# Performance work log

Hardware: AMD Instinct MI355X
Metric: run time of the kernel (lower is better)

Reference implementation:

```python
import jax, jax.numpy as jnp
import numpy as np


def _square_distance(src, dst):
    # src: [B,N,C], dst: [B,M,C] -> [B,N,M] squared euclidean distances
    # ||s-d||^2 = -2 s.d + ||s||^2 + ||d||^2
    d = -2.0 * jnp.einsum('bnc,bmc->bnm', src, dst)
    d = d + jnp.sum(src * src, axis=-1)[:, :, None]
    d = d + jnp.sum(dst * dst, axis=-1)[:, None, :]
    return d


def setup_inputs() -> dict:
    key = jax.random.key(0)
    k1, k2 = jax.random.split(key)
    B, N, M, C = 8, 4096, 4096, 3
    f = jax.random.normal(k1, (B, N, C), dtype=jnp.float32)
    f_ = jax.random.normal(k2, (B, M, C), dtype=jnp.float32)
    return {"f": f, "f_": f_}


def reference(f, f_):
    dis = _square_distance(f, f_)          # [B,N,M]
    f2f_ = jnp.min(dis, axis=2)            # [B,N] nearest in f_ for each f point
    f_2f = jnp.min(dis, axis=1)            # [B,M] nearest in f for each f_ point
    d = jnp.mean(f2f_, axis=1) + jnp.mean(f_2f, axis=1)  # [B]
    return jnp.mean(d)
```

## Files before the change

### kernel.cpp

```cpp
#include <hip/hip_runtime.h>


typedef float v2f __attribute__((ext_vector_type(2)));

constexpr int B = 8;
constexpr int N = 4096;
constexpr int M = 4096;
constexpr int S = 16;
constexpr int TM = M / S;
constexpr int GPS = TM / 2;
constexpr int BLOCK = 256;
constexpr int Q = 4;
constexpr int QPB = BLOCK * Q;
constexpr int QCH = N / QPB;
constexpr int PAIRS = B * (M / 2);

__global__ __launch_bounds__(256) void prep_kernel(
    const float* __restrict__ f,
    const float* __restrict__ f_,
    float* __restrict__ pT0,
    float* __restrict__ pT1,
    unsigned int* __restrict__ minA,
    unsigned int* __restrict__ minB,
    float* __restrict__ out)
{
    const int t = blockIdx.x * 256 + threadIdx.x;
    const int sel = t / PAIRS;
    const int p   = t - sel * PAIRS;
    const float* src = sel ? f : f_;
    float* dst = sel ? pT1 : pT0;

    const float x0 = src[6 * p + 0], y0 = src[6 * p + 1], z0 = src[6 * p + 2];
    const float x1 = src[6 * p + 3], y1 = src[6 * p + 4], z1 = src[6 * p + 5];

    float4 r0, r1;
    r0.x = -2.0f * x0; r0.y = -2.0f * x1;
    r0.z = -2.0f * y0; r0.w = -2.0f * y1;
    r1.x = -2.0f * z0; r1.y = -2.0f * z1;
    r1.z = x0 * x0 + y0 * y0 + z0 * z0;
    r1.w = x1 * x1 + y1 * y1 + z1 * z1;
    ((float4*)dst)[2 * p]     = r0;
    ((float4*)dst)[2 * p + 1] = r1;

    minA[t] = 0x7F800000u;
    minB[t] = 0x7F800000u;

    if (t == 0) out[0] = 0.0f;
}

__global__ __launch_bounds__(256) void chamfer_dir_kernel(
    const float* __restrict__ f,
    const float* __restrict__ f_,
    const float* __restrict__ pT0,
    const float* __restrict__ pT1,
    unsigned int* __restrict__ minA,
    unsigned int* __restrict__ minB)
{
    const int dir = blockIdx.z;
    const int b   = blockIdx.y;
    const int seg = blockIdx.x % S;
    const int qc  = blockIdx.x / S;

    const float* qsrc = dir ? f_ : f;
    const float4* tp  = (const float4*)((dir ? pT1 : pT0)
                        + ((size_t)b * (M / 2) + (size_t)seg * GPS) * 8);
    unsigned int* omin = dir ? minB : minA;

    const int qbase = qc * QPB + threadIdx.x;
    const float* qb = qsrc + (size_t)b * N * 3;

    v2f qxv[Q], qyv[Q], qzv[Q];
    float qn[Q];
    #pragma unroll
    for (int j = 0; j < Q; ++j) {
        const int q = qbase + j * BLOCK;
        const float x = qb[3 * q + 0], y = qb[3 * q + 1], z = qb[3 * q + 2];
        qxv[j] = (v2f){x, x};
        qyv[j] = (v2f){y, y};
        qzv[j] = (v2f){z, z};
        qn[j] = x * x + y * y + z * z;
    }

    float m[Q];
    #pragma unroll
    for (int j = 0; j < Q; ++j) m[j] = 3.402823466e+38f;

    #pragma unroll 4
    for (int g = 0; g < GPS; ++g) {
        const float4 r0 = tp[2 * g];
        const float4 r1 = tp[2 * g + 1];
        const v2f x01 = {r0.x, r0.y};
        const v2f y01 = {r0.z, r0.w};
        const v2f z01 = {r1.x, r1.y};
        const v2f w01 = {r1.z, r1.w};

        #pragma unroll
        for (int j = 0; j < Q; ++j) {
            v2f a = qzv[j] * z01 + w01;
            a = qyv[j] * y01 + a;
            a = qxv[j] * x01 + a;
            m[j] = fminf(fminf(m[j], a.x), a.y);
        }
    }

    #pragma unroll
    for (int j = 0; j < Q; ++j) {
        const float d = m[j] + qn[j];
        atomicMin(&omin[b * N + qbase + j * BLOCK], __float_as_uint(d));
    }
}

__global__ __launch_bounds__(256) void reduce_out_kernel(
    const unsigned int* __restrict__ mins,
    float* __restrict__ out)
{
    __shared__ float wsum[4];
    const int tid = threadIdx.x;
    const int idx = blockIdx.x * 256 + tid;
    float s = 0.f;
    #pragma unroll
    for (int k = 0; k < 4; ++k)
        s += __uint_as_float(mins[idx + k * 16384]);

    #pragma unroll
    for (int off = 32; off > 0; off >>= 1) s += __shfl_down(s, off, 64);
    if ((tid & 63) == 0) wsum[tid >> 6] = s;
    __syncthreads();
    if (tid == 0) {
        float v = (wsum[0] + wsum[1]) + (wsum[2] + wsum[3]);
        atomicAdd(out, v * (1.0f / 32768.0f));
    }
}

extern "C" void kernel_launch(void* const* d_in, const int* in_sizes, int n_in,
                              void* d_out, int out_size, void* d_ws, size_t ws_size,
                              hipStream_t stream) {
    (void)in_sizes; (void)n_in; (void)out_size; (void)ws_size;
    const float* f  = (const float*)d_in[0];
    const float* f_ = (const float*)d_in[1];
    float* out = (float*)d_out;

    unsigned int* minA = (unsigned int*)d_ws;
    unsigned int* minB = minA + (size_t)B * N;
    float* pT0 = (float*)(minB + (size_t)B * M);
    float* pT1 = pT0 + (size_t)PAIRS * 8;

    prep_kernel<<<(2 * PAIRS) / 256, 256, 0, stream>>>(f, f_, pT0, pT1, minA, minB, out);

    dim3 grid(QCH * S, B, 2);
    chamfer_dir_kernel<<<grid, BLOCK, 0, stream>>>(f, f_, pT0, pT1, minA, minB);

    reduce_out_kernel<<<64, 256, 0, stream>>>(minA, out);
}
```

Baseline: 82.30 us.

## Stage target tile in LDS, use packed FMA asm, replace atomics with partial-min buffer

Each block now loads its 2*GPS float4 target tile into shared memory once and reads it from LDS in the inner loop, rather than issuing global loads. The inner distance math is forced onto v_pk_fma_f32 through inline asm. The per-segment atomicMin into global mins is replaced by plain stores into a [dir,B,S,N] partial buffer, and the reduce kernel takes the min over the S segments. This removes atomics and the min-array initialization, at the cost of a larger workspace and more reads in the reduce step.

```diff
diff --git a/kernel.cpp b/kernel.cpp
--- a/kernel.cpp
+++ b/kernel.cpp
@@ -15,13 +15,17 @@
 constexpr int QCH = N / QPB;
 constexpr int PAIRS = B * (M / 2);
 
+__device__ __forceinline__ v2f pk_fma(v2f a, v2f b, v2f c) {
+    v2f d;
+    asm("v_pk_fma_f32 %0, %1, %2, %3" : "=v"(d) : "v"(a), "v"(b), "v"(c));
+    return d;
+}
+
 __global__ __launch_bounds__(256) void prep_kernel(
     const float* __restrict__ f,
     const float* __restrict__ f_,
     float* __restrict__ pT0,
     float* __restrict__ pT1,
-    unsigned int* __restrict__ minA,
-    unsigned int* __restrict__ minB,
     float* __restrict__ out)
 {
     const int t = blockIdx.x * 256 + threadIdx.x;
@@ -42,9 +46,6 @@
     ((float4*)dst)[2 * p]     = r0;
     ((float4*)dst)[2 * p + 1] = r1;
 
-    minA[t] = 0x7F800000u;
-    minB[t] = 0x7F800000u;
-
     if (t == 0) out[0] = 0.0f;
 }
 
@@ -53,22 +54,23 @@
     const float* __restrict__ f_,
     const float* __restrict__ pT0,
     const float* __restrict__ pT1,
-    unsigned int* __restrict__ minA,
-    unsigned int* __restrict__ minB)
+    float* __restrict__ ws2)
 {
+    __shared__ float4 sT[2 * GPS];
+
     const int dir = blockIdx.z;
     const int b   = blockIdx.y;
     const int seg = blockIdx.x % S;
     const int qc  = blockIdx.x / S;
 
     const float* qsrc = dir ? f_ : f;
-    const float4* tp  = (const float4*)((dir ? pT1 : pT0)
+    const float4* tp4 = (const float4*)((dir ? pT1 : pT0)
                         + ((size_t)b * (M / 2) + (size_t)seg * GPS) * 8);
-    unsigned int* omin = dir ? minB : minA;
+
+    sT[threadIdx.x] = tp4[threadIdx.x];
 
     const int qbase = qc * QPB + threadIdx.x;
     const float* qb = qsrc + (size_t)b * N * 3;
-
     v2f qxv[Q], qyv[Q], qzv[Q];
     float qn[Q];
     #pragma unroll
@@ -80,15 +82,16 @@
         qzv[j] = (v2f){z, z};
         qn[j] = x * x + y * y + z * z;
     }
+    __syncthreads();
 
     float m[Q];
     #pragma unroll
     for (int j = 0; j < Q; ++j) m[j] = 3.402823466e+38f;
 
-    #pragma unroll 4
+    #pragma unroll 2
     for (int g = 0; g < GPS; ++g) {
-        const float4 r0 = tp[2 * g];
-        const float4 r1 = tp[2 * g + 1];
+        const float4 r0 = sT[2 * g];
+        const float4 r1 = sT[2 * g + 1];
         const v2f x01 = {r0.x, r0.y};
         const v2f y01 = {r0.z, r0.w};
         const v2f z01 = {r1.x, r1.y};
@@ -96,38 +99,45 @@
 
         #pragma unroll
         for (int j = 0; j < Q; ++j) {
-            v2f a = qzv[j] * z01 + w01;
-            a = qyv[j] * y01 + a;
-            a = qxv[j] * x01 + a;
+            v2f a = pk_fma(qzv[j], z01, w01);
+            a = pk_fma(qyv[j], y01, a);
+            a = pk_fma(qxv[j], x01, a);
             m[j] = fminf(fminf(m[j], a.x), a.y);
         }
     }
 
+    float* row = ws2 + ((size_t)((dir * B + b) * S + seg)) * N;
     #pragma unroll
-    for (int j = 0; j < Q; ++j) {
-        const float d = m[j] + qn[j];
-        atomicMin(&omin[b * N + qbase + j * BLOCK], __float_as_uint(d));
-    }
+    for (int j = 0; j < Q; ++j)
+        row[qbase + j * BLOCK] = m[j] + qn[j];
 }
 
 __global__ __launch_bounds__(256) void reduce_out_kernel(
-    const unsigned int* __restrict__ mins,
+    const float* __restrict__ ws2,
     float* __restrict__ out)
 {
     __shared__ float wsum[4];
     const int tid = threadIdx.x;
-    const int idx = blockIdx.x * 256 + tid;
+    const int t0 = blockIdx.x * 256 + tid;
     float s = 0.f;
     #pragma unroll
-    for (int k = 0; k < 4; ++k)
-        s += __uint_as_float(mins[idx + k * 16384]);
+    for (int j = 0; j < 4; ++j) {
+        const int qid = t0 + j * 16384;
+        const int db  = qid >> 12;
+        const int q   = qid & 4095;
+        const float* rows = ws2 + (size_t)db * S * N + q;
+        float m = rows[0];
+        #pragma unroll
+        for (int sgi = 1; sgi < S; ++sgi) m = fminf(m, rows[(size_t)sgi * N]);
+        s += m;
+    }
 
     #pragma unroll
     for (int off = 32; off > 0; off >>= 1) s += __shfl_down(s, off, 64);
     if ((tid & 63) == 0) wsum[tid >> 6] = s;
     __syncthreads();
     if (tid == 0) {
-        float v = (wsum[0] + wsum[1]) + (wsum[2] + wsum[3]);
+        const float v = (wsum[0] + wsum[1]) + (wsum[2] + wsum[3]);
         atomicAdd(out, v * (1.0f / 32768.0f));
     }
 }
@@ -140,15 +150,14 @@
     const float* f_ = (const float*)d_in[1];
     float* out = (float*)d_out;
 
-    unsigned int* minA = (unsigned int*)d_ws;
-    unsigned int* minB = minA + (size_t)B * N;
-    float* pT0 = (float*)(minB + (size_t)B * M);
+    float* pT0 = (float*)d_ws;
     float* pT1 = pT0 + (size_t)PAIRS * 8;
+    float* ws2 = pT1 + (size_t)PAIRS * 8;
 
-    prep_kernel<<<(2 * PAIRS) / 256, 256, 0, stream>>>(f, f_, pT0, pT1, minA, minB, out);
+    prep_kernel<<<(2 * PAIRS) / 256, 256, 0, stream>>>(f, f_, pT0, pT1, out);
 
     dim3 grid(QCH * S, B, 2);
-    chamfer_dir_kernel<<<grid, BLOCK, 0, stream>>>(f, f_, pT0, pT1, minA, minB);
+    chamfer_dir_kernel<<<grid, BLOCK, 0, stream>>>(f, f_, pT0, pT1, ws2);
 
-    reduce_out_kernel<<<64, 256, 0, stream>>>(minA, out);
+    reduce_out_kernel<<<64, 256, 0, stream>>>(ws2, out);
 }
```

Measured after the change: 81.44 us. Within noise of the previous version (-1.0%).
